# Kernel optimization log

Hardware: AMD Instinct MI355X
Metric: run time of the kernel (lower is better)

## Reference

```python
import jax, jax.numpy as jnp
import numpy as np

N_NODES, IN_DIM, HID, N_CLS, N_T = 4096, 512, 256, 128, 20


def _odefunc(x, A, Wt, bt):
    # X' = relu(Linear(A @ X)); dropout=0.0 so it is the identity
    return jax.nn.relu((A @ x) @ Wt.T + bt)


def _rk4_traj(vt, x0, A, Wt, bt):
    # torchdiffeq 'rk4' = fixed-grid 3/8-rule RK4 stepping between consecutive vt points
    f = lambda y: _odefunc(y, A, Wt, bt)  # autonomous: t unused by ODEFunc

    def step(x, dt):
        k1 = f(x)
        k2 = f(x + dt * k1 / 3.0)
        k3 = f(x + dt * (k2 - k1 / 3.0))
        k4 = f(x + dt * (k1 - k2 + k3))
        xn = x + dt * (k1 + 3.0 * k2 + 3.0 * k3 + k4) / 8.0
        return xn, xn

    dts = vt[1:] - vt[:-1]
    _, ys = jax.lax.scan(step, x0, dts)
    return jnp.concatenate([x0[None], ys], axis=0)  # [T, N, H]


def setup_inputs() -> dict:
    key = jax.random.key(0)
    ks = jax.random.split(key, 8)
    vt = jnp.arange(N_T, dtype=jnp.float32) * 0.05  # increasing time ticks, horizon ~1.0
    x = jax.random.normal(ks[0], (N_NODES, IN_DIM), dtype=jnp.float32)
    # row-scaled dense adjacency (torch.mm dense path); spectral scale ~O(1)
    A = jax.random.uniform(ks[1], (N_NODES, N_NODES), dtype=jnp.float32) / N_NODES
    W1 = jax.random.normal(ks[2], (HID, IN_DIM), dtype=jnp.float32) / np.sqrt(IN_DIM)
    b1 = jnp.zeros((HID,), dtype=jnp.float32)
    W2 = jax.random.normal(ks[3], (HID, HID), dtype=jnp.float32) / np.sqrt(HID)
    b2 = jnp.zeros((HID,), dtype=jnp.float32)
    Wt = jax.random.normal(ks[4], (HID, HID), dtype=jnp.float32) * (0.5 / np.sqrt(HID))
    bt = jnp.zeros((HID,), dtype=jnp.float32)
    Wo = jax.random.normal(ks[5], (N_CLS, HID), dtype=jnp.float32) / np.sqrt(HID)
    bo = jnp.zeros((N_CLS,), dtype=jnp.float32)
    return {"vt": vt, "x": x, "A": A, "W1": W1, "b1": b1, "W2": W2,
            "b2": b2, "Wt": Wt, "bt": bt, "Wo": Wo, "bo": bo}


def reference(vt, x, A, W1, b1, W2, b2, Wt, bt, Wo, bo):
    # input_layer: Linear -> Tanh -> Linear (dropout = 0.0 elsewhere)
    h = jnp.tanh(x @ W1.T + b1) @ W2.T + b2            # [N, H]
    traj = _rk4_traj(vt, h, A, Wt, bt)                 # [T, N, H] (terminal=False -> full trajectory)
    return traj @ Wo.T + bo                            # [T, N, C]
```

## Files before the change

### kernel.cpp

```cpp
#include <hip/hip_runtime.h>
#include <stdint.h>

typedef __bf16 bf16;
typedef bf16 bf16x8 __attribute__((ext_vector_type(8)));
typedef float f32x4 __attribute__((ext_vector_type(4)));
typedef uint32_t u32;
typedef unsigned long long u64;
typedef unsigned char u8;

#define NN   4096
#define HID  256
#define NCLS 128

__device__ __forceinline__ void gload16(const void* g, void* l) {
  __builtin_amdgcn_global_load_lds((const __attribute__((address_space(1))) u32*)g,
                                   (__attribute__((address_space(3))) u32*)l, 16, 0, 0);
}

__global__ void convf2b(const float* __restrict__ s, bf16* __restrict__ d, int n) {
  int i = (blockIdx.x * blockDim.x + threadIdx.x) * 4;
  if (i >= n) return;
  f32x4 v = *(const f32x4*)(s + i);
  bf16 o[4] = {(bf16)v[0], (bf16)v[1], (bf16)v[2], (bf16)v[3]};
  *(u64*)(d + i) = *(u64*)o;
}

__global__ void convAf8(const float* __restrict__ s, u8* __restrict__ d, int n) {
  int i = (blockIdx.x * blockDim.x + threadIdx.x) * 4;
  if (i >= n) return;
  f32x4 v = *(const f32x4*)(s + i);
  u32 pk = __builtin_amdgcn_cvt_pk_fp8_f32(v[0] * 4096.f, v[1] * 4096.f, 0, false);
  pk = __builtin_amdgcn_cvt_pk_fp8_f32(v[2] * 4096.f, v[3] * 4096.f, pk, true);
  *(u32*)(d + i) = pk;
}

__device__ __forceinline__ f32x4 ksplit_reduce(char* smem, f32x4 acc[2][2],
                                               int kw, int sw, int hh, int rl) {
  float* fs = (float*)smem;
  #pragma unroll
  for (int q = 0; q < 4; ++q) {
    const int src = (kw < q) ? kw : kw - 1;
    float* dst = fs + ((q * 3 + src) * 2 + sw) * 272;
    const int mf = q >> 1, nf = q & 1;
    if (q != kw) {
      #pragma unroll
      for (int j = 0; j < 4; ++j) dst[(hh * 4 + j) * 17 + rl] = acc[mf][nf][j];
    }
  }
  asm volatile("s_waitcnt lgkmcnt(0)" ::: "memory");
  __builtin_amdgcn_s_barrier();
  f32x4 r;
  if (kw == 0)      r = acc[0][0];
  else if (kw == 1) r = acc[0][1];
  else if (kw == 2) r = acc[1][0];
  else              r = acc[1][1];
  #pragma unroll
  for (int src = 0; src < 3; ++src) {
    const float* sp = fs + ((kw * 3 + src) * 2 + sw) * 272;
    #pragma unroll
    for (int j = 0; j < 4; ++j) r[j] += sp[(hh * 4 + j) * 17 + rl];
  }
  return r;
}

__global__ __launch_bounds__(512, 2) void gemmf8(
    const u8* __restrict__ Ag,
    const u8* __restrict__ Bg,
    bf16* __restrict__ Cb)
{
  __shared__ __align__(16) char smem[49152];
  const int tid = threadIdx.x;
  const int l = tid & 63, wv = tid >> 6;
  const int kw = wv & 3, sw = wv >> 2;
  const int rl = l & 15, hh = l >> 4;

  const int chunk = gridDim.x >> 3;
  const int sb = (blockIdx.x & 7) * chunk + (blockIdx.x >> 3);
  const int m0 = (sb >> 3) * 64, n0 = (sb & 7) * 32;

  const bool isB = wv >= 4;
  const int w4 = wv & 3;
  const int rlo = l >> 3, gq = l & 7;
  const int sg = gq ^ rlo;
  const int grow = (isB ? n0 + w4 * 8 : m0 + w4 * 16) + rlo;
  const u8* sG = (isB ? Bg : Ag) + (size_t)grow * 4096 + sg * 16;
  const int stoff = isB ? 8192 + w4 * 1024 : w4 * 2048;

  f32x4 acc[2][2];
  #pragma unroll
  for (int i = 0; i < 2; ++i)
    #pragma unroll
    for (int j = 0; j < 2; ++j) acc[i][j] = (f32x4){0.f, 0.f, 0.f, 0.f};

  auto stage = [&](int buf, int t) {
    char* base = smem + buf * 12288 + stoff;
    const u8* g = sG + t * 128;
    gload16(g, base);
    if (!isB) gload16(g + 8 * 4096, base + 1024);
  };

  const int g0 = kw * 2 + (hh >> 1);
  const int co = ((g0 ^ (rl & 7)) << 4) + (hh & 1) * 8;
  auto compute = [&](int buf) {
    const char* As = smem + buf * 12288;
    const char* Bs = As + 8192;
    u64 a0 = *(const u64*)(As + (sw * 32 + rl +  0) * 128 + co);
    u64 a1 = *(const u64*)(As + (sw * 32 + rl + 16) * 128 + co);
    u64 b0 = *(const u64*)(Bs + (rl +  0) * 128 + co);
    u64 b1 = *(const u64*)(Bs + (rl + 16) * 128 + co);
    __builtin_amdgcn_s_setprio(1);
    acc[0][0] = __builtin_amdgcn_mfma_f32_16x16x32_fp8_fp8((long)a0, (long)b0, acc[0][0], 0, 0, 0);
    acc[0][1] = __builtin_amdgcn_mfma_f32_16x16x32_fp8_fp8((long)a0, (long)b1, acc[0][1], 0, 0, 0);
    acc[1][0] = __builtin_amdgcn_mfma_f32_16x16x32_fp8_fp8((long)a1, (long)b0, acc[1][0], 0, 0, 0);
    acc[1][1] = __builtin_amdgcn_mfma_f32_16x16x32_fp8_fp8((long)a1, (long)b1, acc[1][1], 0, 0, 0);
    __builtin_amdgcn_s_setprio(0);
  };

  stage(0, 0); stage(1, 1); stage(2, 2);
  for (int t = 0; t < 32; ++t) {
    const int rem = 31 - t;
    if (rem >= 2) {
      if (!isB) { asm volatile("s_waitcnt vmcnt(4)" ::: "memory"); }
      else      { asm volatile("s_waitcnt vmcnt(2)" ::: "memory"); }
    } else if (rem == 1) {
      if (!isB) { asm volatile("s_waitcnt vmcnt(2)" ::: "memory"); }
      else      { asm volatile("s_waitcnt vmcnt(1)" ::: "memory"); }
    } else       { asm volatile("s_waitcnt vmcnt(0)" ::: "memory"); }
    __builtin_amdgcn_sched_barrier(0);
    __builtin_amdgcn_s_barrier();
    __builtin_amdgcn_sched_barrier(0);
    if (t + 3 < 32) stage((t + 3) & 3, t + 3);
    compute(t & 3);
  }
  __builtin_amdgcn_s_barrier();
  __builtin_amdgcn_sched_barrier(0);

  f32x4 o = ksplit_reduce(smem, acc, kw, sw, hh, rl);
  const int row0 = m0 + sw * 32 + (kw >> 1) * 16 + hh * 4;
  const int col  = n0 + (kw & 1) * 16 + rl;
  #pragma unroll
  for (int r = 0; r < 4; ++r)
    Cb[(row0 + r) * HID + col] = (bf16)(o[r] * 2.44140625e-4f);
}

template<int EPI>
__global__ __launch_bounds__(512, 2) void gemmbf(
    const bf16* __restrict__ Ag, int lda,
    const bf16* __restrict__ Bg, int ldb,
    int Ntiles, int K,
    const float* __restrict__ bias,
    float* __restrict__ outf,
    bf16* __restrict__ outb,
    u8* __restrict__ ybt,
    float* __restrict__ xbuf,
    const float* __restrict__ kk1,
    const float* __restrict__ kk2,
    const float* __restrict__ kk3,
    const float* __restrict__ vt, int step)
{
  __shared__ __align__(16) char smem[49152];
  const int tid = threadIdx.x;
  const int l = tid & 63, wv = tid >> 6;
  const int kw = wv & 3, sw = wv >> 2;
  const int rl = l & 15, hh = l >> 4;

  const int chunk = gridDim.x >> 3;
  const int sb = (blockIdx.x & 7) * chunk + (blockIdx.x >> 3);
  const int mtile = sb / Ntiles;
  const int ntile = sb - mtile * Ntiles;
  const int m0 = mtile * 64, n0 = ntile * 32;

  const bool isB = wv >= 4;
  const int w4 = wv & 3;
  const int rlo = l >> 4, gq = l & 15;
  const size_t ldby = (size_t)(isB ? ldb : lda) * 2;
  const int grow = (isB ? n0 + w4 * 8 : m0 + w4 * 16) + rlo;
  const char* sGb = (const char*)(isB ? (const void*)Bg : (const void*)Ag)
                    + (size_t)grow * ldby;
  const int c0 = (gq ^ rlo) << 4;
  const int c1 = (gq ^ (rlo + 4)) << 4;
  const int stoff = isB ? 16384 + w4 * 2048 : w4 * 4096;

  f32x4 acc[2][2];
  #pragma unroll
  for (int i = 0; i < 2; ++i)
    #pragma unroll
    for (int j = 0; j < 2; ++j) acc[i][j] = (f32x4){0.f, 0.f, 0.f, 0.f};

  auto stage = [&](int buf, int t) {
    char* base = smem + buf * 24576 + stoff;
    const char* g = sGb + (size_t)t * 256;
    gload16(g + c0,            base);
    gload16(g + 4 * ldby + c1, base + 1024);
    if (!isB) {
      gload16(g +  8 * ldby + c0, base + 2048);
      gload16(g + 12 * ldby + c1, base + 3072);
    }
  };

  const int ca = ((kw * 4 + hh) ^ (rl & 7)) << 4;
  auto compute = [&](int buf) {
    const char* As = smem + buf * 24576;
    const char* Bs = As + 16384;
    bf16x8 a0 = *(const bf16x8*)(As + (sw * 32 + rl +  0) * 256 + ca);
    bf16x8 a1 = *(const bf16x8*)(As + (sw * 32 + rl + 16) * 256 + ca);
    bf16x8 b0 = *(const bf16x8*)(Bs + (rl +  0) * 256 + ca);
    bf16x8 b1 = *(const bf16x8*)(Bs + (rl + 16) * 256 + ca);
    __builtin_amdgcn_s_setprio(1);
    acc[0][0] = __builtin_amdgcn_mfma_f32_16x16x32_bf16(a0, b0, acc[0][0], 0, 0, 0);
    acc[0][1] = __builtin_amdgcn_mfma_f32_16x16x32_bf16(a0, b1, acc[0][1], 0, 0, 0);
    acc[1][0] = __builtin_amdgcn_mfma_f32_16x16x32_bf16(a1, b0, acc[1][0], 0, 0, 0);
    acc[1][1] = __builtin_amdgcn_mfma_f32_16x16x32_bf16(a1, b1, acc[1][1], 0, 0, 0);
    __builtin_amdgcn_s_setprio(0);
  };

  const int nmac = K >> 7;
  stage(0, 0);
  asm volatile("s_waitcnt vmcnt(0)" ::: "memory");
  __builtin_amdgcn_s_barrier();
  int cur = 0;
  for (int t = 0; t < nmac; ++t) {
    if (t + 1 < nmac) stage(cur ^ 1, t + 1);
    compute(cur);
    asm volatile("s_waitcnt vmcnt(0)" ::: "memory");
    __builtin_amdgcn_sched_barrier(0);
    __builtin_amdgcn_s_barrier();
    cur ^= 1;
  }
  __builtin_amdgcn_sched_barrier(0);

  f32x4 o = ksplit_reduce(smem, acc, kw, sw, hh, rl);
  const int row0 = m0 + sw * 32 + (kw >> 1) * 16 + hh * 4;
  const int col  = n0 + (kw & 1) * 16 + rl;

  float dtv = 0.f;
  if constexpr (EPI >= 3 && EPI <= 6) dtv = vt[step + 1] - vt[step];

  if constexpr (EPI == 1) {
    #pragma unroll
    for (int r = 0; r < 4; ++r)
      outb[(row0 + r) * HID + col] = (bf16)tanhf(o[r] + bias[col]);
  } else if constexpr (EPI == 2) {
    float yv[4];
    #pragma unroll
    for (int r = 0; r < 4; ++r) {
      float v = o[r] + bias[col];
      xbuf[(row0 + r) * HID + col] = v;
      outb[(row0 + r) * HID + col] = (bf16)v;
      yv[r] = v;
    }
    u32 pk = __builtin_amdgcn_cvt_pk_fp8_f32(yv[0], yv[1], 0, false);
    pk = __builtin_amdgcn_cvt_pk_fp8_f32(yv[2], yv[3], pk, true);
    *(u32*)(ybt + (size_t)col * NN + row0) = pk;
  } else if constexpr (EPI >= 3 && EPI <= 6) {
    float yv[4];
    #pragma unroll
    for (int r = 0; r < 4; ++r) {
      const int idx = (row0 + r) * HID + col;
      float v = fmaxf(o[r] + bias[col], 0.f);
      float xv = xbuf[idx];
      float y;
      if constexpr (EPI == 3)      { outf[idx] = v; y = xv + dtv * (1.f/3.f) * v; }
      else if constexpr (EPI == 4) { outf[idx] = v; y = xv + dtv * (v - kk1[idx] * (1.f/3.f)); }
      else if constexpr (EPI == 5) { outf[idx] = v; y = xv + dtv * (kk1[idx] - kk2[idx] + v); }
      else {
        float xn = xv + dtv * 0.125f * (kk1[idx] + 3.f*kk2[idx] + 3.f*kk3[idx] + v);
        xbuf[idx] = xn;
        outb[idx] = (bf16)xn;
        y = xn;
      }
      yv[r] = y;
    }
    u32 pk = __builtin_amdgcn_cvt_pk_fp8_f32(yv[0], yv[1], 0, false);
    pk = __builtin_amdgcn_cvt_pk_fp8_f32(yv[2], yv[3], pk, true);
    *(u32*)(ybt + (size_t)col * NN + row0) = pk;
  } else {
    #pragma unroll
    for (int r = 0; r < 4; ++r)
      outf[(size_t)(row0 + r) * NCLS + col] = o[r] + bias[col];
  }
}

extern "C" void kernel_launch(void* const* d_in, const int* in_sizes, int n_in,
                              void* d_out, int out_size, void* d_ws, size_t ws_size,
                              hipStream_t stream)
{
  const float* vt = (const float*)d_in[0];
  const float* x  = (const float*)d_in[1];
  const float* A  = (const float*)d_in[2];
  const float* W1 = (const float*)d_in[3];
  const float* b1 = (const float*)d_in[4];
  const float* W2 = (const float*)d_in[5];
  const float* b2 = (const float*)d_in[6];
  const float* Wt = (const float*)d_in[7];
  const float* bt = (const float*)d_in[8];
  const float* Wo = (const float*)d_in[9];
  const float* bo = (const float*)d_in[10];
  float* out = (float*)d_out;

  char* p = (char*)d_ws;
  auto carve = [&](size_t n) { char* r = p; p += (n + 255) & ~(size_t)255; return r; };
  u8*   A8  = (u8*)carve((size_t)4096 * 4096);
  bf16* xb  = (bf16*)carve((size_t)4096 * 512 * 2);
  bf16* W1b = (bf16*)carve((size_t)256 * 512 * 2);
  bf16* W2b = (bf16*)carve((size_t)256 * 256 * 2);
  bf16* Wtb = (bf16*)carve((size_t)256 * 256 * 2);
  bf16* Wob = (bf16*)carve((size_t)128 * 256 * 2);
  bf16* T1b = (bf16*)carve((size_t)4096 * 256 * 2);
  bf16* Cb  = (bf16*)carve((size_t)4096 * 256 * 2);
  u8*   Y8  = (u8*)carve((size_t)256 * 4096);
  float* xs = (float*)carve((size_t)4096 * 256 * 4);
  float* k1 = (float*)carve((size_t)4096 * 256 * 4);
  float* k2 = (float*)carve((size_t)4096 * 256 * 4);
  float* k3 = (float*)carve((size_t)4096 * 256 * 4);
  size_t base_need = (size_t)(p - (char*)d_ws);
  const size_t trajBytes = (size_t)20 * 4096 * 256 * 2;
  bool big = (ws_size >= base_need + trajBytes);
  bf16* traj = (bf16*)carve(big ? trajBytes : (size_t)4096 * 256 * 2);

  convAf8<<<16384, 256, 0, stream>>>(A,  A8,  16777216);
  convf2b<<<2048,  256, 0, stream>>>(x,  xb,  2097152);
  convf2b<<<128,   256, 0, stream>>>(W1, W1b, 131072);
  convf2b<<<64,    256, 0, stream>>>(W2, W2b, 65536);
  convf2b<<<64,    256, 0, stream>>>(Wt, Wtb, 65536);
  convf2b<<<32,    256, 0, stream>>>(Wo, Wob, 32768);

  gemmbf<1><<<512, 512, 0, stream>>>(xb, 512, W1b, 512, 8, 512, b1,
      nullptr, T1b, nullptr, nullptr, nullptr, nullptr, nullptr, vt, 0);
  gemmbf<2><<<512, 512, 0, stream>>>(T1b, 256, W2b, 256, 8, 256, b2,
      nullptr, traj, Y8, xs, nullptr, nullptr, nullptr, vt, 0);
  if (!big)
    gemmbf<7><<<256, 512, 0, stream>>>(traj, 256, Wob, 256, 4, 256, bo,
        out, nullptr, nullptr, nullptr, nullptr, nullptr, nullptr, vt, 0);

  for (int t = 0; t < 19; ++t) {
    bf16* slot = big ? (traj + (size_t)(t + 1) * 4096 * 256) : traj;
    gemmf8<<<512, 512, 0, stream>>>(A8, Y8, Cb);
    gemmbf<3><<<512, 512, 0, stream>>>(Cb, 256, Wtb, 256, 8, 256, bt,
        k1, nullptr, Y8, xs, nullptr, nullptr, nullptr, vt, t);
    gemmf8<<<512, 512, 0, stream>>>(A8, Y8, Cb);
    gemmbf<4><<<512, 512, 0, stream>>>(Cb, 256, Wtb, 256, 8, 256, bt,
        k2, nullptr, Y8, xs, k1, nullptr, nullptr, vt, t);
    gemmf8<<<512, 512, 0, stream>>>(A8, Y8, Cb);
    gemmbf<5><<<512, 512, 0, stream>>>(Cb, 256, Wtb, 256, 8, 256, bt,
        k3, nullptr, Y8, xs, k1, k2, nullptr, vt, t);
    gemmf8<<<512, 512, 0, stream>>>(A8, Y8, Cb);
    gemmbf<6><<<512, 512, 0, stream>>>(Cb, 256, Wtb, 256, 8, 256, bt,
        nullptr, slot, Y8, xs, k1, k2, k3, vt, t);
    if (!big)
      gemmbf<7><<<256, 512, 0, stream>>>(traj, 256, Wob, 256, 4, 256, bo,
          out + (size_t)(t + 1) * 4096 * 128, nullptr, nullptr, nullptr,
          nullptr, nullptr, nullptr, vt, 0);
  }
  if (big)
    gemmbf<7><<<5120, 512, 0, stream>>>(traj, 256, Wob, 256, 4, 256, bo,
        out, nullptr, nullptr, nullptr, nullptr, nullptr, nullptr, vt, 0);
}
```

Before: 1.563 ms.

## Deepen fp8 GEMM prefetch to six buffers and single-shot K=256 bf16 GEMM

The fp8 A@Y kernel moves from a four-buffer ring with three tiles in flight to a six-buffer ring with five tiles prefetched, and its vmcnt waits are adjusted to match. This is meant to hide more global-load latency in the dominant adjacency GEMM, at the cost of more LDS per block (72 KB), which may reduce occupancy below two blocks per CU. The bf16 GEMM gains a compile-time K; for K=256 it loads the whole K slice into LDS in one stage and runs two MFMA k-steps with a single barrier, removing the double-buffered loop overhead.

Result: slower. 1.681 ms (+7.5%).

```diff
diff --git a/kernel.cpp b/kernel.cpp
--- a/kernel.cpp
+++ b/kernel.cpp
@@ -68,7 +68,7 @@
     const u8* __restrict__ Bg,
     bf16* __restrict__ Cb)
 {
-  __shared__ __align__(16) char smem[49152];
+  __shared__ __align__(16) char smem[73728];
   const int tid = threadIdx.x;
   const int l = tid & 63, wv = tid >> 6;
   const int kw = wv & 3, sw = wv >> 2;
@@ -116,21 +116,31 @@
     __builtin_amdgcn_s_setprio(0);
   };
 
-  stage(0, 0); stage(1, 1); stage(2, 2);
+  stage(0, 0); stage(1, 1); stage(2, 2); stage(3, 3); stage(4, 4);
+  int cur = 0, pre = 5;
   for (int t = 0; t < 32; ++t) {
     const int rem = 31 - t;
-    if (rem >= 2) {
-      if (!isB) { asm volatile("s_waitcnt vmcnt(4)" ::: "memory"); }
-      else      { asm volatile("s_waitcnt vmcnt(2)" ::: "memory"); }
-    } else if (rem == 1) {
-      if (!isB) { asm volatile("s_waitcnt vmcnt(2)" ::: "memory"); }
-      else      { asm volatile("s_waitcnt vmcnt(1)" ::: "memory"); }
-    } else       { asm volatile("s_waitcnt vmcnt(0)" ::: "memory"); }
+    const int fut = rem < 4 ? rem : 4;
+    if (!isB) {
+      if (fut == 4)      { asm volatile("s_waitcnt vmcnt(8)" ::: "memory"); }
+      else if (fut == 3) { asm volatile("s_waitcnt vmcnt(6)" ::: "memory"); }
+      else if (fut == 2) { asm volatile("s_waitcnt vmcnt(4)" ::: "memory"); }
+      else if (fut == 1) { asm volatile("s_waitcnt vmcnt(2)" ::: "memory"); }
+      else               { asm volatile("s_waitcnt vmcnt(0)" ::: "memory"); }
+    } else {
+      if (fut == 4)      { asm volatile("s_waitcnt vmcnt(4)" ::: "memory"); }
+      else if (fut == 3) { asm volatile("s_waitcnt vmcnt(3)" ::: "memory"); }
+      else if (fut == 2) { asm volatile("s_waitcnt vmcnt(2)" ::: "memory"); }
+      else if (fut == 1) { asm volatile("s_waitcnt vmcnt(1)" ::: "memory"); }
+      else               { asm volatile("s_waitcnt vmcnt(0)" ::: "memory"); }
+    }
     __builtin_amdgcn_sched_barrier(0);
     __builtin_amdgcn_s_barrier();
     __builtin_amdgcn_sched_barrier(0);
-    if (t + 3 < 32) stage((t + 3) & 3, t + 3);
-    compute(t & 3);
+    if (t + 5 < 32) stage(pre, t + 5);
+    compute(cur);
+    cur = (cur == 5) ? 0 : cur + 1;
+    pre = (pre == 5) ? 0 : pre + 1;
   }
   __builtin_amdgcn_s_barrier();
   __builtin_amdgcn_sched_barrier(0);
@@ -143,11 +153,11 @@
     Cb[(row0 + r) * HID + col] = (bf16)(o[r] * 2.44140625e-4f);
 }
 
-template<int EPI>
+template<int EPI, int KK>
 __global__ __launch_bounds__(512, 2) void gemmbf(
     const bf16* __restrict__ Ag, int lda,
     const bf16* __restrict__ Bg, int ldb,
-    int Ntiles, int K,
+    int Ntiles,
     const float* __restrict__ bias,
     float* __restrict__ outf,
     bf16* __restrict__ outb,
@@ -172,14 +182,6 @@
 
   const bool isB = wv >= 4;
   const int w4 = wv & 3;
-  const int rlo = l >> 4, gq = l & 15;
-  const size_t ldby = (size_t)(isB ? ldb : lda) * 2;
-  const int grow = (isB ? n0 + w4 * 8 : m0 + w4 * 16) + rlo;
-  const char* sGb = (const char*)(isB ? (const void*)Bg : (const void*)Ag)
-                    + (size_t)grow * ldby;
-  const int c0 = (gq ^ rlo) << 4;
-  const int c1 = (gq ^ (rlo + 4)) << 4;
-  const int stoff = isB ? 16384 + w4 * 2048 : w4 * 4096;
 
   f32x4 acc[2][2];
   #pragma unroll
@@ -187,47 +189,102 @@
     #pragma unroll
     for (int j = 0; j < 2; ++j) acc[i][j] = (f32x4){0.f, 0.f, 0.f, 0.f};
 
-  auto stage = [&](int buf, int t) {
-    char* base = smem + buf * 24576 + stoff;
-    const char* g = sGb + (size_t)t * 256;
-    gload16(g + c0,            base);
-    gload16(g + 4 * ldby + c1, base + 1024);
+  if constexpr (KK == 256) {
+    const int lrow = l >> 5, lg = l & 31;
     if (!isB) {
-      gload16(g +  8 * ldby + c0, base + 2048);
-      gload16(g + 12 * ldby + c1, base + 3072);
-    }
-  };
-
-  const int ca = ((kw * 4 + hh) ^ (rl & 7)) << 4;
-  auto compute = [&](int buf) {
-    const char* As = smem + buf * 24576;
-    const char* Bs = As + 16384;
-    bf16x8 a0 = *(const bf16x8*)(As + (sw * 32 + rl +  0) * 256 + ca);
-    bf16x8 a1 = *(const bf16x8*)(As + (sw * 32 + rl + 16) * 256 + ca);
-    bf16x8 b0 = *(const bf16x8*)(Bs + (rl +  0) * 256 + ca);
-    bf16x8 b1 = *(const bf16x8*)(Bs + (rl + 16) * 256 + ca);
-    __builtin_amdgcn_s_setprio(1);
-    acc[0][0] = __builtin_amdgcn_mfma_f32_16x16x32_bf16(a0, b0, acc[0][0], 0, 0, 0);
-    acc[0][1] = __builtin_amdgcn_mfma_f32_16x16x32_bf16(a0, b1, acc[0][1], 0, 0, 0);
-    acc[1][0] = __builtin_amdgcn_mfma_f32_16x16x32_bf16(a1, b0, acc[1][0], 0, 0, 0);
-    acc[1][1] = __builtin_amdgcn_mfma_f32_16x16x32_bf16(a1, b1, acc[1][1], 0, 0, 0);
-    __builtin_amdgcn_s_setprio(0);
-  };
-
-  const int nmac = K >> 7;
-  stage(0, 0);
-  asm volatile("s_waitcnt vmcnt(0)" ::: "memory");
-  __builtin_amdgcn_s_barrier();
-  int cur = 0;
-  for (int t = 0; t < nmac; ++t) {
-    if (t + 1 < nmac) stage(cur ^ 1, t + 1);
-    compute(cur);
+      const char* gb = (const char*)(Ag + (size_t)(m0 + w4 * 16) * lda);
+      char* base = smem + w4 * 8192;
+      #pragma unroll
+      for (int i = 0; i < 8; ++i) {
+        const int r = i * 2 + lrow;
+        const int swz = (lg ^ ((w4 * 16 + r) & 7)) << 4;
+        gload16(gb + (size_t)r * lda * 2 + swz, base + i * 1024);
+      }
+    } else {
+      const char* gb = (const char*)(Bg + (size_t)(n0 + w4 * 8) * ldb);
+      char* base = smem + 32768 + w4 * 4096;
+      #pragma unroll
+      for (int i = 0; i < 4; ++i) {
+        const int r = i * 2 + lrow;
+        const int swz = (lg ^ ((w4 * 8 + r) & 7)) << 4;
+        gload16(gb + (size_t)r * ldb * 2 + swz, base + i * 1024);
+      }
+    }
     asm volatile("s_waitcnt vmcnt(0)" ::: "memory");
     __builtin_amdgcn_sched_barrier(0);
     __builtin_amdgcn_s_barrier();
-    cur ^= 1;
-  }
-  __builtin_amdgcn_sched_barrier(0);
+    __builtin_amdgcn_sched_barrier(0);
+
+    const char* As = smem;
+    const char* Bs = smem + 32768;
+    #pragma unroll
+    for (int ks = 0; ks < 2; ++ks) {
+      const int ca = ((((kw * 2 + ks) * 4 + hh) ^ (rl & 7)) << 4);
+      bf16x8 a0 = *(const bf16x8*)(As + (sw * 32 + rl +  0) * 512 + ca);
+      bf16x8 a1 = *(const bf16x8*)(As + (sw * 32 + rl + 16) * 512 + ca);
+      bf16x8 b0 = *(const bf16x8*)(Bs + (rl +  0) * 512 + ca);
+      bf16x8 b1 = *(const bf16x8*)(Bs + (rl + 16) * 512 + ca);
+      __builtin_amdgcn_s_setprio(1);
+      acc[0][0] = __builtin_amdgcn_mfma_f32_16x16x32_bf16(a0, b0, acc[0][0], 0, 0, 0);
+      acc[0][1] = __builtin_amdgcn_mfma_f32_16x16x32_bf16(a0, b1, acc[0][1], 0, 0, 0);
+      acc[1][0] = __builtin_amdgcn_mfma_f32_16x16x32_bf16(a1, b0, acc[1][0], 0, 0, 0);
+      acc[1][1] = __builtin_amdgcn_mfma_f32_16x16x32_bf16(a1, b1, acc[1][1], 0, 0, 0);
+      __builtin_amdgcn_s_setprio(0);
+    }
+    __builtin_amdgcn_s_barrier();
+    __builtin_amdgcn_sched_barrier(0);
+  } else {
+    const int rlo = l >> 4, gq = l & 15;
+    const size_t ldby = (size_t)(isB ? ldb : lda) * 2;
+    const int grow = (isB ? n0 + w4 * 8 : m0 + w4 * 16) + rlo;
+    const char* sGb = (const char*)(isB ? (const void*)Bg : (const void*)Ag)
+                      + (size_t)grow * ldby;
+    const int c0 = (gq ^ rlo) << 4;
+    const int c1 = (gq ^ (rlo + 4)) << 4;
+    const int stoff = isB ? 16384 + w4 * 2048 : w4 * 4096;
+
+    auto stage = [&](int buf, int t) {
+      char* base = smem + buf * 24576 + stoff;
+      const char* g = sGb + (size_t)t * 256;
+      gload16(g + c0,            base);
+      gload16(g + 4 * ldby + c1, base + 1024);
+      if (!isB) {
+        gload16(g +  8 * ldby + c0, base + 2048);
+        gload16(g + 12 * ldby + c1, base + 3072);
+      }
+    };
+
+    const int ca = ((kw * 4 + hh) ^ (rl & 7)) << 4;
+    auto compute = [&](int buf) {
+      const char* As = smem + buf * 24576;
+      const char* Bs = As + 16384;
+      bf16x8 a0 = *(const bf16x8*)(As + (sw * 32 + rl +  0) * 256 + ca);
+      bf16x8 a1 = *(const bf16x8*)(As + (sw * 32 + rl + 16) * 256 + ca);
+      bf16x8 b0 = *(const bf16x8*)(Bs + (rl +  0) * 256 + ca);
+      bf16x8 b1 = *(const bf16x8*)(Bs + (rl + 16) * 256 + ca);
+      __builtin_amdgcn_s_setprio(1);
+      acc[0][0] = __builtin_amdgcn_mfma_f32_16x16x32_bf16(a0, b0, acc[0][0], 0, 0, 0);
+      acc[0][1] = __builtin_amdgcn_mfma_f32_16x16x32_bf16(a0, b1, acc[0][1], 0, 0, 0);
+      acc[1][0] = __builtin_amdgcn_mfma_f32_16x16x32_bf16(a1, b0, acc[1][0], 0, 0, 0);
+      acc[1][1] = __builtin_amdgcn_mfma_f32_16x16x32_bf16(a1, b1, acc[1][1], 0, 0, 0);
+      __builtin_amdgcn_s_setprio(0);
+    };
+
+    const int nmac = KK >> 7;
+    stage(0, 0);
+    asm volatile("s_waitcnt vmcnt(0)" ::: "memory");
+    __builtin_amdgcn_s_barrier();
+    int cur = 0;
+    for (int t = 0; t < nmac; ++t) {
+      if (t + 1 < nmac) stage(cur ^ 1, t + 1);
+      compute(cur);
+      asm volatile("s_waitcnt vmcnt(0)" ::: "memory");
+      __builtin_amdgcn_sched_barrier(0);
+      __builtin_amdgcn_s_barrier();
+      cur ^= 1;
+    }
+    __builtin_amdgcn_sched_barrier(0);
+  }
 
   f32x4 o = ksplit_reduce(smem, acc, kw, sw, hh, rl);
   const int row0 = m0 + sw * 32 + (kw >> 1) * 16 + hh * 4;
@@ -325,34 +382,34 @@
   convf2b<<<64,    256, 0, stream>>>(Wt, Wtb, 65536);
   convf2b<<<32,    256, 0, stream>>>(Wo, Wob, 32768);
 
-  gemmbf<1><<<512, 512, 0, stream>>>(xb, 512, W1b, 512, 8, 512, b1,
+  gemmbf<1, 512><<<512, 512, 0, stream>>>(xb, 512, W1b, 512, 8, b1,
       nullptr, T1b, nullptr, nullptr, nullptr, nullptr, nullptr, vt, 0);
-  gemmbf<2><<<512, 512, 0, stream>>>(T1b, 256, W2b, 256, 8, 256, b2,
+  gemmbf<2, 256><<<512, 512, 0, stream>>>(T1b, 256, W2b, 256, 8, b2,
       nullptr, traj, Y8, xs, nullptr, nullptr, nullptr, vt, 0);
   if (!big)
-    gemmbf<7><<<256, 512, 0, stream>>>(traj, 256, Wob, 256, 4, 256, bo,
+    gemmbf<7, 256><<<256, 512, 0, stream>>>(traj, 256, Wob, 256, 4, bo,
         out, nullptr, nullptr, nullptr, nullptr, nullptr, nullptr, vt, 0);
 
   for (int t = 0; t < 19; ++t) {
     bf16* slot = big ? (traj + (size_t)(t + 1) * 4096 * 256) : traj;
     gemmf8<<<512, 512, 0, stream>>>(A8, Y8, Cb);
-    gemmbf<3><<<512, 512, 0, stream>>>(Cb, 256, Wtb, 256, 8, 256, bt,
+    gemmbf<3, 256><<<512, 512, 0, stream>>>(Cb, 256, Wtb, 256, 8, bt,
         k1, nullptr, Y8, xs, nullptr, nullptr, nullptr, vt, t);
     gemmf8<<<512, 512, 0, stream>>>(A8, Y8, Cb);
-    gemmbf<4><<<512, 512, 0, stream>>>(Cb, 256, Wtb, 256, 8, 256, bt,
+    gemmbf<4, 256><<<512, 512, 0, stream>>>(Cb, 256, Wtb, 256, 8, bt,
         k2, nullptr, Y8, xs, k1, nullptr, nullptr, vt, t);
     gemmf8<<<512, 512, 0, stream>>>(A8, Y8, Cb);
-    gemmbf<5><<<512, 512, 0, stream>>>(Cb, 256, Wtb, 256, 8, 256, bt,
+    gemmbf<5, 256><<<512, 512, 0, stream>>>(Cb, 256, Wtb, 256, 8, bt,
         k3, nullptr, Y8, xs, k1, k2, nullptr, vt, t);
     gemmf8<<<512, 512, 0, stream>>>(A8, Y8, Cb);
-    gemmbf<6><<<512, 512, 0, stream>>>(Cb, 256, Wtb, 256, 8, 256, bt,
+    gemmbf<6, 256><<<512, 512, 0, stream>>>(Cb, 256, Wtb, 256, 8, bt,
         nullptr, slot, Y8, xs, k1, k2, k3, vt, t);
     if (!big)
-      gemmbf<7><<<256, 512, 0, stream>>>(traj, 256, Wob, 256, 4, 256, bo,
+      gemmbf<7, 256><<<256, 512, 0, stream>>>(traj, 256, Wob, 256, 4, bo,
           out + (size_t)(t + 1) * 4096 * 128, nullptr, nullptr, nullptr,
           nullptr, nullptr, nullptr, vt, 0);
   }
   if (big)
-    gemmbf<7><<<5120, 512, 0, stream>>>(traj, 256, Wob, 256, 4, 256, bo,
+    gemmbf<7, 256><<<5120, 512, 0, stream>>>(traj, 256, Wob, 256, 4, bo,
         out, nullptr, nullptr, nullptr, nullptr, nullptr, nullptr, vt, 0);
 }
```

## Double FP8 GEMM K-tile to 256 and use three-stage pipeline

Applied to the files above, without the earlier changes.

The FP8 adjacency GEMM now loads 256-byte K slices per stage instead of 128, halving the loop trip count and the barriers per output. Each iteration issues two MFMA groups. The pipeline changes from four buffers with a prefetch distance of three to three buffers with a prefetch distance of two. Shared memory grows to 72KB, which may limit occupancy to fewer blocks per CU than the launch bounds of two request, and the shallower prefetch may expose more load latency.

After: 1.468 ms. 1.06x faster.

```diff
diff --git a/kernel.cpp b/kernel.cpp
--- a/kernel.cpp
+++ b/kernel.cpp
@@ -68,7 +68,7 @@
     const u8* __restrict__ Bg,
     bf16* __restrict__ Cb)
 {
-  __shared__ __align__(16) char smem[49152];
+  __shared__ __align__(16) char smem[73728];
   const int tid = threadIdx.x;
   const int l = tid & 63, wv = tid >> 6;
   const int kw = wv & 3, sw = wv >> 2;
@@ -80,11 +80,13 @@
 
   const bool isB = wv >= 4;
   const int w4 = wv & 3;
-  const int rlo = l >> 3, gq = l & 7;
-  const int sg = gq ^ rlo;
-  const int grow = (isB ? n0 + w4 * 8 : m0 + w4 * 16) + rlo;
-  const u8* sG = (isB ? Bg : Ag) + (size_t)grow * 4096 + sg * 16;
-  const int stoff = isB ? 8192 + w4 * 1024 : w4 * 2048;
+  const int rlo = l >> 4;
+  const int gq = l & 15;
+  const int rowbase = isB ? n0 + w4 * 8 : m0 + w4 * 16;
+  const u8* sGbase = (isB ? Bg : Ag) + (size_t)rowbase * 4096;
+  const int c0 = (gq ^ rlo) << 4;
+  const int c1 = (gq ^ (rlo + 4)) << 4;
+  const int stoff = isB ? 16384 + w4 * 2048 : w4 * 4096;
 
   f32x4 acc[2][2];
   #pragma unroll
@@ -93,44 +95,50 @@
     for (int j = 0; j < 2; ++j) acc[i][j] = (f32x4){0.f, 0.f, 0.f, 0.f};
 
   auto stage = [&](int buf, int t) {
-    char* base = smem + buf * 12288 + stoff;
-    const u8* g = sG + t * 128;
-    gload16(g, base);
-    if (!isB) gload16(g + 8 * 4096, base + 1024);
+    char* base = smem + buf * 24576 + stoff;
+    const u8* g = sGbase + (size_t)rlo * 4096 + t * 256;
+    gload16(g + c0,                      base);
+    gload16(g + (size_t)4  * 4096 + c1,  base + 1024);
+    if (!isB) {
+      gload16(g + (size_t)8  * 4096 + c0, base + 2048);
+      gload16(g + (size_t)12 * 4096 + c1, base + 3072);
+    }
   };
 
-  const int g0 = kw * 2 + (hh >> 1);
-  const int co = ((g0 ^ (rl & 7)) << 4) + (hh & 1) * 8;
   auto compute = [&](int buf) {
-    const char* As = smem + buf * 12288;
-    const char* Bs = As + 8192;
-    u64 a0 = *(const u64*)(As + (sw * 32 + rl +  0) * 128 + co);
-    u64 a1 = *(const u64*)(As + (sw * 32 + rl + 16) * 128 + co);
-    u64 b0 = *(const u64*)(Bs + (rl +  0) * 128 + co);
-    u64 b1 = *(const u64*)(Bs + (rl + 16) * 128 + co);
-    __builtin_amdgcn_s_setprio(1);
-    acc[0][0] = __builtin_amdgcn_mfma_f32_16x16x32_fp8_fp8((long)a0, (long)b0, acc[0][0], 0, 0, 0);
-    acc[0][1] = __builtin_amdgcn_mfma_f32_16x16x32_fp8_fp8((long)a0, (long)b1, acc[0][1], 0, 0, 0);
-    acc[1][0] = __builtin_amdgcn_mfma_f32_16x16x32_fp8_fp8((long)a1, (long)b0, acc[1][0], 0, 0, 0);
-    acc[1][1] = __builtin_amdgcn_mfma_f32_16x16x32_fp8_fp8((long)a1, (long)b1, acc[1][1], 0, 0, 0);
-    __builtin_amdgcn_s_setprio(0);
+    const char* As = smem + buf * 24576;
+    const char* Bs = As + 16384;
+    #pragma unroll
+    for (int ks = 0; ks < 2; ++ks) {
+      const int g0 = (kw * 2 + ks) * 2 + (hh >> 1);
+      const int co = ((g0 ^ (rl & 7)) << 4) + (hh & 1) * 8;
+      u64 a0 = *(const u64*)(As + (sw * 32 + rl +  0) * 256 + co);
+      u64 a1 = *(const u64*)(As + (sw * 32 + rl + 16) * 256 + co);
+      u64 b0 = *(const u64*)(Bs + (rl +  0) * 256 + co);
+      u64 b1 = *(const u64*)(Bs + (rl + 16) * 256 + co);
+      __builtin_amdgcn_s_setprio(1);
+      acc[0][0] = __builtin_amdgcn_mfma_f32_16x16x32_fp8_fp8((long)a0, (long)b0, acc[0][0], 0, 0, 0);
+      acc[0][1] = __builtin_amdgcn_mfma_f32_16x16x32_fp8_fp8((long)a0, (long)b1, acc[0][1], 0, 0, 0);
+      acc[1][0] = __builtin_amdgcn_mfma_f32_16x16x32_fp8_fp8((long)a1, (long)b0, acc[1][0], 0, 0, 0);
+      acc[1][1] = __builtin_amdgcn_mfma_f32_16x16x32_fp8_fp8((long)a1, (long)b1, acc[1][1], 0, 0, 0);
+      __builtin_amdgcn_s_setprio(0);
+    }
   };
 
-  stage(0, 0); stage(1, 1); stage(2, 2);
-  for (int t = 0; t < 32; ++t) {
-    const int rem = 31 - t;
-    if (rem >= 2) {
+  stage(0, 0); stage(1, 1);
+  int cur = 0, pre = 2;
+  for (int t = 0; t < 16; ++t) {
+    if (t < 15) {
       if (!isB) { asm volatile("s_waitcnt vmcnt(4)" ::: "memory"); }
       else      { asm volatile("s_waitcnt vmcnt(2)" ::: "memory"); }
-    } else if (rem == 1) {
-      if (!isB) { asm volatile("s_waitcnt vmcnt(2)" ::: "memory"); }
-      else      { asm volatile("s_waitcnt vmcnt(1)" ::: "memory"); }
     } else       { asm volatile("s_waitcnt vmcnt(0)" ::: "memory"); }
     __builtin_amdgcn_sched_barrier(0);
     __builtin_amdgcn_s_barrier();
     __builtin_amdgcn_sched_barrier(0);
-    if (t + 3 < 32) stage((t + 3) & 3, t + 3);
-    compute(t & 3);
+    if (t + 2 < 16) stage(pre, t + 2);
+    compute(cur);
+    cur = (cur == 2) ? 0 : cur + 1;
+    pre = (pre == 2) ? 0 : pre + 1;
   }
   __builtin_amdgcn_s_barrier();
   __builtin_amdgcn_sched_barrier(0);
```
